# Performance work log

Measured on AMD Instinct MI355X. Metric: run time of the kernel, lower is better.

## Reference

```python
import jax, jax.numpy as jnp
import numpy as np

B, C, P, E, M, H, K = 1024, 8192, 3, 64, 128, 16, 8
SCALE = 0.05
EPS = 1e-12  # tf.math.l2_normalize epsilon


def setup_inputs() -> dict:
    key = jax.random.key(0)
    ks = jax.random.split(key, 16)
    return {
        'pools': jax.random.uniform(ks[0], (B, C), dtype=jnp.float32),            # dense stand-in for SparseTensor batch_pools
        'metapaths': jax.random.uniform(ks[1], (P, C, C), dtype=jnp.float32),     # card-card metapath matrices
        'card_embeddings': jax.random.normal(ks[2], (C, E), dtype=jnp.float32) * SCALE,
        'mp_kernels': jax.random.normal(ks[3], (P, E, M), dtype=jnp.float32) * SCALE,
        'mp_biases': jnp.zeros((P, M, 1), dtype=jnp.float32),
        'Wq': jax.random.normal(ks[4], (M, H, K), dtype=jnp.float32) * SCALE,
        'bq': jnp.zeros((H, K), dtype=jnp.float32),
        'Wk': jax.random.normal(ks[5], (M, H, K), dtype=jnp.float32) * SCALE,
        'bk': jnp.zeros((H, K), dtype=jnp.float32),
        'Wv': jax.random.normal(ks[6], (M, H, K), dtype=jnp.float32) * SCALE,
        'bv': jnp.zeros((H, K), dtype=jnp.float32),
        'Wo': jax.random.normal(ks[7], (H, K, M), dtype=jnp.float32) * SCALE,
        'bo': jnp.zeros((M,), dtype=jnp.float32),
        'pool_kernel': jax.random.normal(ks[8], (M, E), dtype=jnp.float32) * SCALE,
        'pool_bias': jnp.zeros((E,), dtype=jnp.float32),
    }


def _l2_normalize(x, axis):
    # matches tf.math.l2_normalize: x / sqrt(max(sum(x^2), eps))
    sq = jnp.sum(jnp.square(x), axis=axis, keepdims=True)
    return x * jax.lax.rsqrt(jnp.maximum(sq, EPS))


def reference(pools, metapaths, card_embeddings, mp_kernels, mp_biases,
              Wq, bq, Wk, bk, Wv, bv, Wo, bo, pool_kernel, pool_bias):
    # --- MetapathEmbed layers, vectorized over the P metapaths ---
    # path_card_embeddings: act(einsum('ce,em->mc') + bias) -> (P, M, C)
    path_card = jax.nn.silu(jnp.einsum('ce,pem->pmc', card_embeddings, mp_kernels) + mp_biases)
    # path_card_matrix: einsum('mc,cd->dm') -> (P, C, M)
    pcm = jnp.einsum('pmc,pcd->pdm', path_card, metapaths)
    # sparse_dense_matmul(batch_pools, path_card_matrix); stack over metapaths -> (B, P, M)
    x = jnp.einsum('bd,pdm->bpm', pools, pcm)

    # --- keras MultiHeadAttention(query=x, value=x) ---
    q = jnp.einsum('bpm,mhk->bphk', x, Wq) + bq
    k = jnp.einsum('bpm,mhk->bphk', x, Wk) + bk
    v = jnp.einsum('bpm,mhk->bphk', x, Wv) + bv
    scores = jnp.einsum('bphk,bqhk->bhpq', q, k) / np.float32(np.sqrt(K))
    attn = jax.nn.softmax(scores, axis=-1)
    o = jnp.einsum('bhpq,bqhk->bphk', attn, v)
    attended = jnp.einsum('bphk,hkm->bpm', o, Wo) + bo  # (B, P, M)

    # --- pooling head ---
    pre_pool = jnp.sum(attended, axis=1)                       # (B, M)
    pool_embeds = jnp.einsum('bm,me->be', pre_pool, pool_kernel) + pool_bias
    norm_pool = _l2_normalize(pool_embeds, axis=1)             # (B, E)
    norm_cards = _l2_normalize(card_embeddings, axis=1)        # (C, E)
    return (jnp.einsum('be,ce->bc', norm_pool, norm_cards) + 1.0) / 2.0
```

## Files before the change

### kernel.cpp

```cpp
#include <hip/hip_runtime.h>
#include <hip/hip_bf16.h>

typedef unsigned int uint;
typedef unsigned short ushort;
typedef float f32x4 __attribute__((ext_vector_type(4)));
typedef short s16x8 __attribute__((ext_vector_type(8)));
typedef int i32x4 __attribute__((ext_vector_type(4)));
typedef uint u32x2 __attribute__((ext_vector_type(2)));

#define C_DIM 8192
#define B_DIM 1024
#define P_DIM 3
#define E_DIM 64
#define M_DIM 128

#define PCA_OFF   0ull
#define PART_OFF  15728640ull
#define PCMH_OFF  66060288ull
#define PCML_OFF  72351744ull
#define XPART_OFF PART_OFF
#define NPOOL_OFF 78643200ull
#define NCARD_OFF 78774272ull

__device__ __forceinline__ uint bf16_rne(float f) {
  uint u = __builtin_bit_cast(uint, f);
  return (u + 0x7fffu + ((u >> 16) & 1u)) >> 16;
}
__device__ __forceinline__ float bf16_to_f32(uint b) {
  return __builtin_bit_cast(float, b << 16);
}
__device__ __forceinline__ uint pk2(float a, float b) {
  float2 t; t.x = a; t.y = b;
  __hip_bfloat162 h2 = __float22bfloat162_rn(t);
  uint r;
  __builtin_memcpy(&r, &h2, 4);
  return r;
}

__global__ __launch_bounds__(256) void k1_pathcard(
    const float* __restrict__ cardemb, const float* __restrict__ mpk,
    const float* __restrict__ mpbias, ushort* __restrict__ pcA) {
  __shared__ float ce_l[64 * 68];
  const int tid = threadIdx.x;
  const int cb = blockIdx.x;
  const int p  = blockIdx.y;
  for (int r = 0; r < 16; ++r) {
    int i = r * 256 + tid;
    int row = i >> 6, col = i & 63;
    ce_l[row * 68 + col] = cardemb[(size_t)(cb * 64 + row) * 64 + col];
  }
  __syncthreads();
  const int m = tid & 127;
  const int chalf = tid >> 7;
  float kr[64];
#pragma unroll
  for (int e = 0; e < 64; ++e) kr[e] = mpk[(size_t)p * E_DIM * M_DIM + e * M_DIM + m];
  const float bias = mpbias[p * M_DIM + m];
  for (int cl0 = 0; cl0 < 32; ++cl0) {
    int cl = chalf * 32 + cl0;
    float acc = bias;
#pragma unroll
    for (int e = 0; e < 64; ++e) acc += ce_l[cl * 68 + e] * kr[e];
    float s = acc / (1.0f + expf(-acc));
    uint hb = bf16_rne(s);
    uint lb = bf16_rne(s - bf16_to_f32(hb));
    int c = cb * 64 + cl;
    int kt = c >> 5, kl = c & 31;
    size_t off = ((size_t)(p * 256 + kt) * 20480 + (size_t)m * 80 + (size_t)kl * 2) >> 1;
    pcA[off] = (ushort)hb;
    pcA[off + 5120] = (ushort)lb;
  }
}

__global__ __launch_bounds__(256, 3) void k2_big(
    const float* __restrict__ mp, const ushort* __restrict__ pcA,
    float* __restrict__ partial) {
  __shared__ char smem[32768];
  const int tid = threadIdx.x;
  int lin = blockIdx.x + 64 * (blockIdx.y + 4 * blockIdx.z);
  int swz = (lin & 7) * 96 + (lin >> 3);
  const int dt = swz & 63, q = (swz >> 6) & 3, p = swz >> 8;
  const int lane = tid & 63, wid = tid >> 6;
  const int wr = wid >> 1, wc = wid & 1;
  const int r16 = lane & 15, g4 = lane >> 4;
  const float* mpb = mp + (size_t)p * C_DIM * C_DIM + (size_t)dt * 128;
  const char* pcb = (const char*)pcA + (size_t)(p * 256 + q * 64) * 20480;
  const int sd = tid & 127, skh = tid >> 7;
  const int fc = ((sd ^ (sd >> 2)) & 3) << 4;
  const int fr = ((r16 ^ (r16 >> 2)) & 3) << 4;

  f32x4 acc[4][4];
#pragma unroll
  for (int i = 0; i < 4; ++i)
#pragma unroll
    for (int j = 0; j < 4; ++j) acc[i][j] = (f32x4){0.f, 0.f, 0.f, 0.f};

  float brA[16], brB[16];
  s16x8 ah[4], al[4];

#define LOADA(T)                                                              \
  {                                                                           \
    const char* At_ = pcb + (size_t)(T) * 20480;                              \
    _Pragma("unroll") for (int i = 0; i < 4; ++i) {                           \
      int offa_ = (wr * 64 + i * 16 + r16) * 80 + g4 * 16;                    \
      ah[i] = *(const s16x8*)(At_ + offa_);                                   \
      al[i] = *(const s16x8*)(At_ + 10240 + offa_);                           \
    }                                                                         \
  }

#define LOADB(T, BR)                                                          \
  {                                                                           \
    int c0_ = q * 2048 + (T) * 32;                                            \
    _Pragma("unroll") for (int ii = 0; ii < 2; ++ii) {                        \
      const float* rp_ = mpb + (size_t)(c0_ + ii * 16 + skh * 8) * C_DIM + sd;\
      _Pragma("unroll") for (int j = 0; j < 8; ++j)                           \
          BR[ii * 8 + j] = rp_[(size_t)j * C_DIM];                            \
    }                                                                         \
  }

#define WRITEB(BR, BUF)                                                       \
  {                                                                           \
    char* bb_ = smem + (BUF) * 16384;                                         \
    _Pragma("unroll") for (int ii = 0; ii < 2; ++ii) {                        \
      uint hw_[4], lw_[4];                                                    \
      _Pragma("unroll") for (int k2 = 0; k2 < 4; ++k2) {                      \
        float v0_ = BR[ii * 8 + k2 * 2], v1_ = BR[ii * 8 + k2 * 2 + 1];       \
        uint h_ = pk2(v0_, v1_);                                              \
        float h0_ = __builtin_bit_cast(float, h_ << 16);                      \
        float h1_ = __builtin_bit_cast(float, h_ & 0xffff0000u);              \
        hw_[k2] = h_;                                                         \
        lw_[k2] = pk2(v0_ - h0_, v1_ - h1_);                                  \
      }                                                                       \
      int off_ = sd * 64 + ((((ii * 2 + skh) << 4)) ^ fc);                    \
      *(i32x4*)(bb_ + off_) =                                                 \
          (i32x4){(int)hw_[0], (int)hw_[1], (int)hw_[2], (int)hw_[3]};        \
      *(i32x4*)(bb_ + 8192 + off_) =                                          \
          (i32x4){(int)lw_[0], (int)lw_[1], (int)lw_[2], (int)lw_[3]};        \
    }                                                                         \
  }

#define MFMAB(BUF)                                                            \
  {                                                                           \
    const char* Bb_ = smem + (BUF) * 16384;                                   \
    _Pragma("unroll") for (int j = 0; j < 4; ++j) {                           \
      int offb_ = (wc * 64 + j * 16 + r16) * 64 + ((g4 << 4) ^ fr);           \
      s16x8 bh_ = *(const s16x8*)(Bb_ + offb_);                               \
      s16x8 bl_ = *(const s16x8*)(Bb_ + 8192 + offb_);                        \
      _Pragma("unroll") for (int i = 0; i < 4; ++i) {                         \
        acc[i][j] =                                                           \
            __builtin_amdgcn_mfma_f32_16x16x32_bf16(ah[i], bh_, acc[i][j], 0, 0, 0); \
        acc[i][j] =                                                           \
            __builtin_amdgcn_mfma_f32_16x16x32_bf16(ah[i], bl_, acc[i][j], 0, 0, 0); \
        acc[i][j] =                                                           \
            __builtin_amdgcn_mfma_f32_16x16x32_bf16(al[i], bh_, acc[i][j], 0, 0, 0); \
      }                                                                       \
    }                                                                         \
  }

  LOADB(0, brA);
  LOADB(1, brB);
  WRITEB(brA, 0);
  asm volatile("s_waitcnt lgkmcnt(0)" ::: "memory");
  __builtin_amdgcn_s_barrier();
  __builtin_amdgcn_sched_barrier(0);

#define K2S(T, BRL, BRW, TAIL)                                                \
  {                                                                           \
    LOADA(T);                                                                 \
    asm volatile("" ::: "memory");                                            \
    if ((T) < 62) LOADB((T) + 2, BRL);                                        \
    MFMAB((T) & 1);                                                           \
    if (!(TAIL)) {                                                            \
      WRITEB(BRW, ((T) + 1) & 1);                                             \
      asm volatile("s_waitcnt lgkmcnt(0)" ::: "memory");                      \
      __builtin_amdgcn_s_barrier();                                           \
      __builtin_amdgcn_sched_barrier(0);                                      \
    }                                                                         \
  }

  for (int t2 = 0; t2 < 32; ++t2) {
    int t = 2 * t2;
    K2S(t, brA, brB, false);
    K2S(t + 1, brB, brA, (t2 == 31));
  }
#undef K2S
#undef MFMAB
#undef WRITEB
#undef LOADB
#undef LOADA

  float* part = partial + (size_t)(q * 3 + p) * M_DIM * C_DIM + (size_t)dt * 128;
#pragma unroll
  for (int i = 0; i < 4; ++i)
#pragma unroll
    for (int j = 0; j < 4; ++j)
#pragma unroll
      for (int r = 0; r < 4; ++r)
        part[(size_t)(wr * 64 + i * 16 + g4 * 4 + r) * C_DIM + (wc * 64 + j * 16 + r16)] =
            acc[i][j][r];
}

__global__ __launch_bounds__(256) void k2b_reduce(const float* __restrict__ p0,
                                                  ushort* __restrict__ oh,
                                                  ushort* __restrict__ ol) {
  size_t i = (size_t)blockIdx.x * 256 + threadIdx.x;
  f32x4 a = *(const f32x4*)(p0 + i * 4);
  f32x4 b = *(const f32x4*)(p0 + 3145728ull + i * 4);
  f32x4 c = *(const f32x4*)(p0 + 6291456ull + i * 4);
  f32x4 d = *(const f32x4*)(p0 + 9437184ull + i * 4);
  f32x4 s = (a + b) + (c + d);
  uint h[2], l[2];
#pragma unroll
  for (int k = 0; k < 2; ++k) {
    float v0 = s[k * 2], v1 = s[k * 2 + 1];
    uint hh = pk2(v0, v1);
    float h0 = __builtin_bit_cast(float, hh << 16);
    float h1 = __builtin_bit_cast(float, hh & 0xffff0000u);
    h[k] = hh;
    l[k] = pk2(v0 - h0, v1 - h1);
  }
  *(u32x2*)(oh + i * 4) = (u32x2){h[0], h[1]};
  *(u32x2*)(ol + i * 4) = (u32x2){l[0], l[1]};
}

__global__ __launch_bounds__(256, 2) void k3_x(const float* __restrict__ pools,
                                               const ushort* __restrict__ pcmh,
                                               const ushort* __restrict__ pcml,
                                               float* __restrict__ xpart) {
  const int tid = threadIdx.x;
  const int bt = blockIdx.x, ks = blockIdx.y;
  const int lane = tid & 63, w = tid >> 6;
  const int r16 = lane & 15, g4 = lane >> 4;
  const int rowbase = bt * 32;
  f32x4 acc[2][6];
#pragma unroll
  for (int i = 0; i < 2; ++i)
#pragma unroll
    for (int j = 0; j < 6; ++j) acc[i][j] = (f32x4){0.f, 0.f, 0.f, 0.f};

  f32x4 pv0[2], pv1[2];
#pragma unroll
  for (int i = 0; i < 2; ++i) {
    const float* ap = pools + (size_t)(rowbase + i * 16 + r16) * C_DIM + ks * 512 + g4 * 8;
    pv0[i] = *(const f32x4*)ap;
    pv1[i] = *(const f32x4*)(ap + 4);
  }

  for (int t = 0; t < 16; ++t) {
    int d0 = ks * 512 + t * 32 + g4 * 8;
    s16x8 ah[2], al[2];
#pragma unroll
    for (int i = 0; i < 2; ++i) {
      i32x4 hw, lw;
#pragma unroll
      for (int k2 = 0; k2 < 4; ++k2) {
        float x0 = (k2 < 2) ? pv0[i][k2 * 2] : pv1[i][(k2 - 2) * 2];
        float x1 = (k2 < 2) ? pv0[i][k2 * 2 + 1] : pv1[i][(k2 - 2) * 2 + 1];
        uint h = pk2(x0, x1);
        float h0 = __builtin_bit_cast(float, h << 16);
        float h1 = __builtin_bit_cast(float, h & 0xffff0000u);
        hw[k2] = (int)h;
        lw[k2] = (int)pk2(x0 - h0, x1 - h1);
      }
      ah[i] = __builtin_bit_cast(s16x8, hw);
      al[i] = __builtin_bit_cast(s16x8, lw);
    }
    if (t < 15) {
#pragma unroll
      for (int i = 0; i < 2; ++i) {
        const float* ap =
            pools + (size_t)(rowbase + i * 16 + r16) * C_DIM + d0 + 32;
        pv0[i] = *(const f32x4*)ap;
        pv1[i] = *(const f32x4*)(ap + 4);
      }
    }
#pragma unroll
    for (int j = 0; j < 6; ++j) {
      int col = w * 96 + j * 16 + r16;
      size_t boff = (size_t)col * C_DIM + d0;
      s16x8 bh = *(const s16x8*)(pcmh + boff);
      s16x8 bl = *(const s16x8*)(pcml + boff);
#pragma unroll
      for (int i = 0; i < 2; ++i) {
        acc[i][j] = __builtin_amdgcn_mfma_f32_16x16x32_bf16(ah[i], bh, acc[i][j], 0, 0, 0);
        acc[i][j] = __builtin_amdgcn_mfma_f32_16x16x32_bf16(ah[i], bl, acc[i][j], 0, 0, 0);
        acc[i][j] = __builtin_amdgcn_mfma_f32_16x16x32_bf16(al[i], bh, acc[i][j], 0, 0, 0);
      }
    }
  }
#pragma unroll
  for (int i = 0; i < 2; ++i)
#pragma unroll
    for (int j = 0; j < 6; ++j)
#pragma unroll
      for (int r = 0; r < 4; ++r) {
        int row = rowbase + i * 16 + g4 * 4 + r;
        int col = w * 96 + j * 16 + r16;
        int p = col >> 7, m = col & 127;
        xpart[((size_t)(ks * B_DIM + row) * 3 + p) * M_DIM + m] = acc[i][j][r];
      }
}

__global__ __launch_bounds__(128) void k4_attn(
    const float* __restrict__ xpart, const float* __restrict__ Wq,
    const float* __restrict__ bq, const float* __restrict__ Wk,
    const float* __restrict__ bk, const float* __restrict__ Wv,
    const float* __restrict__ bv, const float* __restrict__ Wo,
    const float* __restrict__ bo, const float* __restrict__ pk,
    const float* __restrict__ pb, ushort* __restrict__ npool) {
  __shared__ float xs[3 * 128], qa[3 * 128], ka[3 * 128], va[3 * 128], oa[3 * 128], pp[128];
  const int t = threadIdx.x;
  const int b = blockIdx.x;
#pragma unroll
  for (int p = 0; p < 3; ++p) {
    float v = 0.f;
    for (int ks = 0; ks < 16; ++ks)
      v += xpart[((size_t)(ks * B_DIM + b) * 3 + p) * M_DIM + t];
    xs[p * 128 + t] = v;
  }
  __syncthreads();
  float qv[3], kv[3], vv[3];
#pragma unroll
  for (int p = 0; p < 3; ++p) { qv[p] = bq[t]; kv[p] = bk[t]; vv[p] = bv[t]; }
  for (int m = 0; m < 128; ++m) {
    float wq = Wq[m * 128 + t], wk = Wk[m * 128 + t], wv = Wv[m * 128 + t];
#pragma unroll
    for (int p = 0; p < 3; ++p) {
      float xv = xs[p * 128 + m];
      qv[p] += xv * wq;
      kv[p] += xv * wk;
      vv[p] += xv * wv;
    }
  }
#pragma unroll
  for (int p = 0; p < 3; ++p) {
    qa[p * 128 + t] = qv[p];
    ka[p * 128 + t] = kv[p];
    va[p * 128 + t] = vv[p];
  }
  __syncthreads();
  const int h = t >> 3;
  float w[3][3];
#pragma unroll
  for (int p = 0; p < 3; ++p) {
    float s[3];
#pragma unroll
    for (int qq = 0; qq < 3; ++qq) {
      float d = 0.f;
#pragma unroll
      for (int kk = 0; kk < 8; ++kk)
        d += qa[p * 128 + h * 8 + kk] * ka[qq * 128 + h * 8 + kk];
      s[qq] = d / 2.8284271247461903f;
    }
    float mx = fmaxf(s[0], fmaxf(s[1], s[2]));
    float e0 = expf(s[0] - mx), e1 = expf(s[1] - mx), e2 = expf(s[2] - mx);
    float inv = 1.0f / (e0 + e1 + e2);
    w[p][0] = e0 * inv; w[p][1] = e1 * inv; w[p][2] = e2 * inv;
  }
#pragma unroll
  for (int p = 0; p < 3; ++p) {
    float o = w[p][0] * va[0 * 128 + t] + w[p][1] * va[1 * 128 + t] + w[p][2] * va[2 * 128 + t];
    oa[p * 128 + t] = o;
  }
  __syncthreads();
  float pre = 3.0f * bo[t];
#pragma unroll
  for (int p = 0; p < 3; ++p)
    for (int hk = 0; hk < 128; ++hk) pre += oa[p * 128 + hk] * Wo[hk * 128 + t];
  pp[t] = pre;
  __syncthreads();
  if (t < 64) {
    float pe = pb[t];
    for (int m = 0; m < 128; ++m) pe += pp[m] * pk[m * 64 + t];
    float ss = pe * pe;
#pragma unroll
    for (int off = 32; off; off >>= 1) ss += __shfl_xor(ss, off, 64);
    float rs = 1.0f / sqrtf(fmaxf(ss, 1e-12f));
    npool[b * 64 + t] = (ushort)bf16_rne(pe * rs);
  }
}

__global__ __launch_bounds__(256) void k4b_ncard(const float* __restrict__ ce,
                                                 ushort* __restrict__ ncard) {
  const int t = threadIdx.x;
  const int r = blockIdx.x * 4 + (t >> 6);
  const int lane = t & 63;
  float v = ce[(size_t)r * 64 + lane];
  float ss = v * v;
#pragma unroll
  for (int off = 32; off; off >>= 1) ss += __shfl_xor(ss, off, 64);
  float rs = 1.0f / sqrtf(fmaxf(ss, 1e-12f));
  ncard[(size_t)r * 64 + lane] = (ushort)bf16_rne(v * rs);
}

__global__ __launch_bounds__(256, 2) void k5_out(const ushort* __restrict__ np_,
                                                 const ushort* __restrict__ nc,
                                                 float* __restrict__ out) {
  const int tid = threadIdx.x;
  const int bt = blockIdx.x, ct = blockIdx.y;
  const int lane = tid & 63, wid = tid >> 6;
  const int wr = wid >> 1, wc = wid & 1;
  const int r16 = lane & 15, g4 = lane >> 4;
  f32x4 acc[4][4];
#pragma unroll
  for (int i = 0; i < 4; ++i)
#pragma unroll
    for (int j = 0; j < 4; ++j) acc[i][j] = (f32x4){0.f, 0.f, 0.f, 0.f};
#pragma unroll
  for (int ks = 0; ks < 2; ++ks) {
    int e0 = ks * 32 + g4 * 8;
    s16x8 af[4], bf_[4];
#pragma unroll
    for (int i = 0; i < 4; ++i)
      af[i] = *(const s16x8*)(np_ + (size_t)(bt * 128 + wr * 64 + i * 16 + r16) * 64 + e0);
#pragma unroll
    for (int j = 0; j < 4; ++j)
      bf_[j] = *(const s16x8*)(nc + (size_t)(ct * 128 + wc * 64 + j * 16 + r16) * 64 + e0);
#pragma unroll
    for (int i = 0; i < 4; ++i)
#pragma unroll
      for (int j = 0; j < 4; ++j)
        acc[i][j] = __builtin_amdgcn_mfma_f32_16x16x32_bf16(af[i], bf_[j], acc[i][j], 0, 0, 0);
  }
#pragma unroll
  for (int i = 0; i < 4; ++i)
#pragma unroll
    for (int j = 0; j < 4; ++j)
#pragma unroll
      for (int r = 0; r < 4; ++r) {
        int row = bt * 128 + wr * 64 + i * 16 + g4 * 4 + r;
        int col = ct * 128 + wc * 64 + j * 16 + r16;
        out[(size_t)row * C_DIM + col] = (acc[i][j][r] + 1.0f) * 0.5f;
      }
}

extern "C" void kernel_launch(void* const* d_in, const int* in_sizes, int n_in,
                              void* d_out, int out_size, void* d_ws, size_t ws_size,
                              hipStream_t stream) {
  const float* pools = (const float*)d_in[0];
  const float* metapaths = (const float*)d_in[1];
  const float* cardemb = (const float*)d_in[2];
  const float* mpk = (const float*)d_in[3];
  const float* mpbias = (const float*)d_in[4];
  const float* Wq = (const float*)d_in[5];
  const float* bq = (const float*)d_in[6];
  const float* Wk = (const float*)d_in[7];
  const float* bk = (const float*)d_in[8];
  const float* Wv = (const float*)d_in[9];
  const float* bv = (const float*)d_in[10];
  const float* Wo = (const float*)d_in[11];
  const float* bo = (const float*)d_in[12];
  const float* pk = (const float*)d_in[13];
  const float* pb = (const float*)d_in[14];
  float* out = (float*)d_out;
  char* ws = (char*)d_ws;

  ushort* pcA = (ushort*)(ws + PCA_OFF);
  float* part = (float*)(ws + PART_OFF);
  ushort* pcmh = (ushort*)(ws + PCMH_OFF);
  ushort* pcml = (ushort*)(ws + PCML_OFF);
  float* xpart = (float*)(ws + XPART_OFF);
  ushort* npool = (ushort*)(ws + NPOOL_OFF);
  ushort* ncard = (ushort*)(ws + NCARD_OFF);

  k1_pathcard<<<dim3(128, 3), dim3(256), 0, stream>>>(cardemb, mpk, mpbias, pcA);
  k2_big<<<dim3(64, 4, 3), dim3(256), 0, stream>>>(metapaths, pcA, part);
  k2b_reduce<<<dim3(3072), dim3(256), 0, stream>>>(part, pcmh, pcml);
  k3_x<<<dim3(32, 16), dim3(256), 0, stream>>>(pools, pcmh, pcml, xpart);
  k4b_ncard<<<dim3(2048), dim3(256), 0, stream>>>(cardemb, ncard);
  k4_attn<<<dim3(1024), dim3(128), 0, stream>>>(xpart, Wq, bq, Wk, bk, Wv, bv, Wo, bo, pk, pb,
                                                npool);
  k5_out<<<dim3(8, 64), dim3(256), 0, stream>>>(npool, ncard, out);
}
```

Before: 353.4 us.

## Reorder k2 pipeline to double-buffer A fragments and halve k3 row tile

In the big metapath GEMM kernel, the software pipeline is restructured. The A-operand register fragments are now double-buffered and loaded one step ahead. The B-tile staging uses a single register set written to shared memory right after the MFMA block, so loads overlap with compute differently. Separately, the pools×pcm kernel now handles 16 rows per block instead of 32, with twice as many blocks and a launch bound of 4 waves per SIMD. This raises occupancy at the cost of reloading the B operand twice as often from global memory.

```diff
diff --git a/kernel.cpp b/kernel.cpp
--- a/kernel.cpp
+++ b/kernel.cpp
@@ -95,36 +95,34 @@
 #pragma unroll
     for (int j = 0; j < 4; ++j) acc[i][j] = (f32x4){0.f, 0.f, 0.f, 0.f};
 
-  float brA[16], brB[16];
-  s16x8 ah[4], al[4];
-
-#define LOADA(T)                                                              \
+  float br[16];
+  s16x8 ahA[4], alA[4], ahB[4], alB[4];
+
+#define LOADA(T, AH, AL)                                                      \
   {                                                                           \
     const char* At_ = pcb + (size_t)(T) * 20480;                              \
     _Pragma("unroll") for (int i = 0; i < 4; ++i) {                           \
       int offa_ = (wr * 64 + i * 16 + r16) * 80 + g4 * 16;                    \
-      ah[i] = *(const s16x8*)(At_ + offa_);                                   \
-      al[i] = *(const s16x8*)(At_ + 10240 + offa_);                           \
+      AH[i] = *(const s16x8*)(At_ + offa_);                                   \
+      AL[i] = *(const s16x8*)(At_ + 10240 + offa_);                           \
     }                                                                         \
   }
-
-#define LOADB(T, BR)                                                          \
+#define LOADB(T)                                                              \
   {                                                                           \
     int c0_ = q * 2048 + (T) * 32;                                            \
     _Pragma("unroll") for (int ii = 0; ii < 2; ++ii) {                        \
       const float* rp_ = mpb + (size_t)(c0_ + ii * 16 + skh * 8) * C_DIM + sd;\
       _Pragma("unroll") for (int j = 0; j < 8; ++j)                           \
-          BR[ii * 8 + j] = rp_[(size_t)j * C_DIM];                            \
+          br[ii * 8 + j] = rp_[(size_t)j * C_DIM];                            \
     }                                                                         \
   }
-
-#define WRITEB(BR, BUF)                                                       \
+#define WRITEB(BUF)                                                           \
   {                                                                           \
     char* bb_ = smem + (BUF) * 16384;                                         \
     _Pragma("unroll") for (int ii = 0; ii < 2; ++ii) {                        \
       uint hw_[4], lw_[4];                                                    \
       _Pragma("unroll") for (int k2 = 0; k2 < 4; ++k2) {                      \
-        float v0_ = BR[ii * 8 + k2 * 2], v1_ = BR[ii * 8 + k2 * 2 + 1];       \
+        float v0_ = br[ii * 8 + k2 * 2], v1_ = br[ii * 8 + k2 * 2 + 1];       \
         uint h_ = pk2(v0_, v1_);                                              \
         float h0_ = __builtin_bit_cast(float, h_ << 16);                      \
         float h1_ = __builtin_bit_cast(float, h_ & 0xffff0000u);              \
@@ -138,8 +136,7 @@
           (i32x4){(int)lw_[0], (int)lw_[1], (int)lw_[2], (int)lw_[3]};        \
     }                                                                         \
   }
-
-#define MFMAB(BUF)                                                            \
+#define MFMAB(BUF, AH, AL)                                                    \
   {                                                                           \
     const char* Bb_ = smem + (BUF) * 16384;                                   \
     _Pragma("unroll") for (int j = 0; j < 4; ++j) {                           \
@@ -148,30 +145,32 @@
       s16x8 bl_ = *(const s16x8*)(Bb_ + 8192 + offb_);                        \
       _Pragma("unroll") for (int i = 0; i < 4; ++i) {                         \
         acc[i][j] =                                                           \
-            __builtin_amdgcn_mfma_f32_16x16x32_bf16(ah[i], bh_, acc[i][j], 0, 0, 0); \
+            __builtin_amdgcn_mfma_f32_16x16x32_bf16(AH[i], bh_, acc[i][j], 0, 0, 0); \
         acc[i][j] =                                                           \
-            __builtin_amdgcn_mfma_f32_16x16x32_bf16(ah[i], bl_, acc[i][j], 0, 0, 0); \
+            __builtin_amdgcn_mfma_f32_16x16x32_bf16(AH[i], bl_, acc[i][j], 0, 0, 0); \
         acc[i][j] =                                                           \
-            __builtin_amdgcn_mfma_f32_16x16x32_bf16(al[i], bh_, acc[i][j], 0, 0, 0); \
+            __builtin_amdgcn_mfma_f32_16x16x32_bf16(AL[i], bh_, acc[i][j], 0, 0, 0); \
       }                                                                       \
     }                                                                         \
   }
 
-  LOADB(0, brA);
-  LOADB(1, brB);
-  WRITEB(brA, 0);
+  LOADA(0, ahA, alA);
+  asm volatile("" ::: "memory");
+  LOADB(0);
+  WRITEB(0);
+  LOADB(1);
   asm volatile("s_waitcnt lgkmcnt(0)" ::: "memory");
   __builtin_amdgcn_s_barrier();
   __builtin_amdgcn_sched_barrier(0);
 
-#define K2S(T, BRL, BRW, TAIL)                                                \
+#define K2S(T, AHC, ALC, AHN, ALN)                                            \
   {                                                                           \
-    LOADA(T);                                                                 \
-    asm volatile("" ::: "memory");                                            \
-    if ((T) < 62) LOADB((T) + 2, BRL);                                        \
-    MFMAB((T) & 1);                                                           \
-    if (!(TAIL)) {                                                            \
-      WRITEB(BRW, ((T) + 1) & 1);                                             \
+    MFMAB((T) & 1, AHC, ALC);                                                 \
+    if ((T) < 63) {                                                           \
+      WRITEB(((T) + 1) & 1);                                                  \
+      LOADA((T) + 1, AHN, ALN);                                               \
+      asm volatile("" ::: "memory");                                          \
+      if ((T) + 2 < 64) LOADB((T) + 2);                                       \
       asm volatile("s_waitcnt lgkmcnt(0)" ::: "memory");                      \
       __builtin_amdgcn_s_barrier();                                           \
       __builtin_amdgcn_sched_barrier(0);                                      \
@@ -180,8 +179,8 @@
 
   for (int t2 = 0; t2 < 32; ++t2) {
     int t = 2 * t2;
-    K2S(t, brA, brB, false);
-    K2S(t + 1, brB, brA, (t2 == 31));
+    K2S(t, ahA, alA, ahB, alB);
+    K2S(t + 1, ahB, alB, ahA, alA);
   }
 #undef K2S
 #undef MFMAB
@@ -223,7 +222,7 @@
   *(u32x2*)(ol + i * 4) = (u32x2){l[0], l[1]};
 }
 
-__global__ __launch_bounds__(256, 2) void k3_x(const float* __restrict__ pools,
+__global__ __launch_bounds__(256, 4) void k3_x(const float* __restrict__ pools,
                                                const ushort* __restrict__ pcmh,
                                                const ushort* __restrict__ pcml,
                                                float* __restrict__ xpart) {
@@ -231,48 +230,40 @@
   const int bt = blockIdx.x, ks = blockIdx.y;
   const int lane = tid & 63, w = tid >> 6;
   const int r16 = lane & 15, g4 = lane >> 4;
-  const int rowbase = bt * 32;
-  f32x4 acc[2][6];
-#pragma unroll
-  for (int i = 0; i < 2; ++i)
-#pragma unroll
-    for (int j = 0; j < 6; ++j) acc[i][j] = (f32x4){0.f, 0.f, 0.f, 0.f};
-
-  f32x4 pv0[2], pv1[2];
-#pragma unroll
-  for (int i = 0; i < 2; ++i) {
-    const float* ap = pools + (size_t)(rowbase + i * 16 + r16) * C_DIM + ks * 512 + g4 * 8;
-    pv0[i] = *(const f32x4*)ap;
-    pv1[i] = *(const f32x4*)(ap + 4);
+  const int rowbase = bt * 16;
+  f32x4 acc[6];
+#pragma unroll
+  for (int j = 0; j < 6; ++j) acc[j] = (f32x4){0.f, 0.f, 0.f, 0.f};
+
+  f32x4 pv0, pv1;
+  {
+    const float* ap = pools + (size_t)(rowbase + r16) * C_DIM + ks * 512 + g4 * 8;
+    pv0 = *(const f32x4*)ap;
+    pv1 = *(const f32x4*)(ap + 4);
   }
 
   for (int t = 0; t < 16; ++t) {
     int d0 = ks * 512 + t * 32 + g4 * 8;
-    s16x8 ah[2], al[2];
-#pragma unroll
-    for (int i = 0; i < 2; ++i) {
+    s16x8 ah, al;
+    {
       i32x4 hw, lw;
 #pragma unroll
       for (int k2 = 0; k2 < 4; ++k2) {
-        float x0 = (k2 < 2) ? pv0[i][k2 * 2] : pv1[i][(k2 - 2) * 2];
-        float x1 = (k2 < 2) ? pv0[i][k2 * 2 + 1] : pv1[i][(k2 - 2) * 2 + 1];
+        float x0 = (k2 < 2) ? pv0[k2 * 2] : pv1[(k2 - 2) * 2];
+        float x1 = (k2 < 2) ? pv0[k2 * 2 + 1] : pv1[(k2 - 2) * 2 + 1];
         uint h = pk2(x0, x1);
         float h0 = __builtin_bit_cast(float, h << 16);
         float h1 = __builtin_bit_cast(float, h & 0xffff0000u);
         hw[k2] = (int)h;
         lw[k2] = (int)pk2(x0 - h0, x1 - h1);
       }
-      ah[i] = __builtin_bit_cast(s16x8, hw);
-      al[i] = __builtin_bit_cast(s16x8, lw);
+      ah = __builtin_bit_cast(s16x8, hw);
+      al = __builtin_bit_cast(s16x8, lw);
     }
     if (t < 15) {
-#pragma unroll
-      for (int i = 0; i < 2; ++i) {
-        const float* ap =
-            pools + (size_t)(rowbase + i * 16 + r16) * C_DIM + d0 + 32;
-        pv0[i] = *(const f32x4*)ap;
-        pv1[i] = *(const f32x4*)(ap + 4);
-      }
+      const float* ap = pools + (size_t)(rowbase + r16) * C_DIM + d0 + 32;
+      pv0 = *(const f32x4*)ap;
+      pv1 = *(const f32x4*)(ap + 4);
     }
 #pragma unroll
     for (int j = 0; j < 6; ++j) {
@@ -280,25 +271,20 @@
       size_t boff = (size_t)col * C_DIM + d0;
       s16x8 bh = *(const s16x8*)(pcmh + boff);
       s16x8 bl = *(const s16x8*)(pcml + boff);
-#pragma unroll
-      for (int i = 0; i < 2; ++i) {
-        acc[i][j] = __builtin_amdgcn_mfma_f32_16x16x32_bf16(ah[i], bh, acc[i][j], 0, 0, 0);
-        acc[i][j] = __builtin_amdgcn_mfma_f32_16x16x32_bf16(ah[i], bl, acc[i][j], 0, 0, 0);
-        acc[i][j] = __builtin_amdgcn_mfma_f32_16x16x32_bf16(al[i], bh, acc[i][j], 0, 0, 0);
-      }
-    }
-  }
-#pragma unroll
-  for (int i = 0; i < 2; ++i)
-#pragma unroll
-    for (int j = 0; j < 6; ++j)
-#pragma unroll
-      for (int r = 0; r < 4; ++r) {
-        int row = rowbase + i * 16 + g4 * 4 + r;
-        int col = w * 96 + j * 16 + r16;
-        int p = col >> 7, m = col & 127;
-        xpart[((size_t)(ks * B_DIM + row) * 3 + p) * M_DIM + m] = acc[i][j][r];
-      }
+      acc[j] = __builtin_amdgcn_mfma_f32_16x16x32_bf16(ah, bh, acc[j], 0, 0, 0);
+      acc[j] = __builtin_amdgcn_mfma_f32_16x16x32_bf16(ah, bl, acc[j], 0, 0, 0);
+      acc[j] = __builtin_amdgcn_mfma_f32_16x16x32_bf16(al, bh, acc[j], 0, 0, 0);
+    }
+  }
+#pragma unroll
+  for (int j = 0; j < 6; ++j)
+#pragma unroll
+    for (int r = 0; r < 4; ++r) {
+      int row = rowbase + g4 * 4 + r;
+      int col = w * 96 + j * 16 + r16;
+      int p = col >> 7, m = col & 127;
+      xpart[((size_t)(ks * B_DIM + row) * 3 + p) * M_DIM + m] = acc[j][r];
+    }
 }
 
 __global__ __launch_bounds__(128) void k4_attn(
@@ -466,7 +452,7 @@
   k1_pathcard<<<dim3(128, 3), dim3(256), 0, stream>>>(cardemb, mpk, mpbias, pcA);
   k2_big<<<dim3(64, 4, 3), dim3(256), 0, stream>>>(metapaths, pcA, part);
   k2b_reduce<<<dim3(3072), dim3(256), 0, stream>>>(part, pcmh, pcml);
-  k3_x<<<dim3(32, 16), dim3(256), 0, stream>>>(pools, pcmh, pcml, xpart);
+  k3_x<<<dim3(64, 16), dim3(256), 0, stream>>>(pools, pcmh, pcml, xpart);
   k4b_ncard<<<dim3(2048), dim3(256), 0, stream>>>(cardemb, ncard);
   k4_attn<<<dim3(1024), dim3(128), 0, stream>>>(xpart, Wq, bq, Wk, bk, Wv, bv, Wo, bo, pk, pb,
                                                 npool);
```

Result: slower. 406.3 us (+15.0%).
